# Kernel tuning notes

Hardware: AMD Instinct MI355X
Metric: run time of the kernel (lower is better)

Reference implementation:

```python
import jax, jax.numpy as jnp
import numpy as np

B, N, C = 4, 4096, 1024
H, M = 16, 64          # num_heads, num_landmarks
DH = C // H
SCALE = H ** (-0.5)    # faithful to source: num_heads**-0.5
LN_EPS = 1e-5


def setup_inputs() -> dict:
    key = jax.random.key(0)
    ks = jax.random.split(key, 8)
    s = 0.02
    return {
        "x": jax.random.normal(ks[0], (B, N, C), jnp.float32),
        "ln_w": jnp.ones((C,), jnp.float32),
        "ln_b": jnp.zeros((C,), jnp.float32),
        "qkv_w": jax.random.normal(ks[1], (3 * C, C), jnp.float32) * s,
        "qkv_b": jax.random.normal(ks[2], (3 * C,), jnp.float32) * s,
        "gamma_w": jax.random.normal(ks[3], (C, C), jnp.float32) * s,
        "gamma_b": jax.random.normal(ks[4], (C,), jnp.float32) * s,
        "proj_w": jax.random.normal(ks[5], (C, C), jnp.float32) * s,
        "proj_b": jax.random.normal(ks[6], (C,), jnp.float32) * s,
    }


def _iterative_inv(K, n_iter=6):
    # Newton-Schulz pseudo-inverse on [..., M, M]
    Id = jnp.eye(K.shape[-1], dtype=K.dtype)
    KA = jnp.abs(K)
    V0 = KA.sum(axis=-2, keepdims=True).max(axis=-1, keepdims=True)
    VI = KA.sum(axis=-1, keepdims=True).max(axis=-2, keepdims=True)
    V = jnp.swapaxes(K, -2, -1) / (V0 * VI)
    for _ in range(n_iter):
        KV = K @ V
        V = 0.25 * V @ (13.0 * Id - KV @ (15.0 * Id - KV @ (7.0 * Id - KV)))
    return V


def reference(x, ln_w, ln_b, qkv_w, qkv_b, gamma_w, gamma_b, proj_w, proj_b):
    # LayerNorm
    mu = x.mean(axis=-1, keepdims=True)
    var = x.var(axis=-1, keepdims=True)
    xn = (x - mu) * jax.lax.rsqrt(var + LN_EPS) * ln_w + ln_b
    # qkv: (B,N,3C) -> (3,B,H,N,DH)
    qkv = (xn @ qkv_w.T + qkv_b).reshape(B, N, 3, H, DH).transpose(2, 0, 3, 1, 4)
    q, k, v = qkv[0], qkv[1], qkv[2]
    # landmarks: mean-pool segments of length N//M, then scale
    q_lm = q.reshape(B, H, M, N // M, DH).mean(axis=-2) * SCALE  # (B,H,M,DH)
    k_lm = k.reshape(B, H, M, N // M, DH).mean(axis=-2) * SCALE
    attn1 = jax.nn.softmax(jnp.einsum('bhnd,bhmd->bhnm', q, k_lm), axis=-1)    # (B,H,N,M)
    attn2 = jax.nn.softmax(jnp.einsum('bhmd,bhld->bhml', q_lm, k_lm), axis=-1)  # (B,H,M,M)
    attn3 = jax.nn.softmax(jnp.einsum('bhmd,bhnd->bhmn', q_lm, k), axis=-1)    # (B,H,M,N)
    attn2_inv = _iterative_inv(attn2)
    out = attn1 @ (attn2_inv @ (attn3 @ v))            # (B,H,N,DH)
    out = out.transpose(0, 2, 1, 3).reshape(B, N, C)
    out = out @ gamma_w.T + gamma_b                    # LipNorm=True branch
    out = out @ proj_w.T + proj_b                      # proj (dropout p=0 is identity)
    return out
```

## Files before the change

kernel.cpp:

```cpp
#include <hip/hip_runtime.h>
#include <stdint.h>

typedef unsigned short u16;
typedef short bf16x8 __attribute__((ext_vector_type(8)));
typedef float f32x4 __attribute__((ext_vector_type(4)));

#define MFMA16(a, b, c) __builtin_amdgcn_mfma_f32_16x16x32_bf16((a), (b), (c), 0, 0, 0)

static __device__ __forceinline__ float bfu2f(u16 u) {
  union { unsigned int i; float f; } z; z.i = ((unsigned int)u) << 16; return z.f;
}
static __device__ __forceinline__ u16 f2bfu(float f) {
  union { float f; unsigned int i; } z; z.f = f;
  unsigned int i = z.i;
  return (u16)((i + 0x7fffu + ((i >> 16) & 1u)) >> 16);
}

__device__ __forceinline__ void gload_lds16(const void* g, void* l) {
  __builtin_amdgcn_global_load_lds((const __attribute__((address_space(1))) void*)g,
                                   (__attribute__((address_space(3))) void*)l, 16, 0, 0);
}

__global__ __launch_bounds__(256) void prep_kernel(
    const float* __restrict__ x, const float* __restrict__ lw,
    const float* __restrict__ lb, u16* __restrict__ xn,
    const float* __restrict__ qkvw, u16* __restrict__ QKVW,
    const float* __restrict__ projw, u16* __restrict__ PW,
    const float* __restrict__ G, u16* __restrict__ GT) {
  int blk = blockIdx.x;
  int t = threadIdx.x;
  if (blk < 16384) {
    int row = blk;
    const float4* xr = (const float4*)(x + (size_t)row * 1024);
    float4 v = xr[t];
    float s = v.x + v.y + v.z + v.w;
    float ss = v.x * v.x + v.y * v.y + v.z * v.z + v.w * v.w;
#pragma unroll
    for (int m = 1; m < 64; m <<= 1) { s += __shfl_xor(s, m); ss += __shfl_xor(ss, m); }
    __shared__ float sb[4], ssb[4];
    int lane = t & 63, wvi = t >> 6;
    if (lane == 0) { sb[wvi] = s; ssb[wvi] = ss; }
    __syncthreads();
    s = sb[0] + sb[1] + sb[2] + sb[3];
    ss = ssb[0] + ssb[1] + ssb[2] + ssb[3];
    float mu = s * (1.0f / 1024.0f);
    float var = ss * (1.0f / 1024.0f) - mu * mu;
    float rstd = rsqrtf(var + 1e-5f);
    float4 wv4 = ((const float4*)lw)[t];
    float4 bv4 = ((const float4*)lb)[t];
    ushort4 o;
    o.x = f2bfu((v.x - mu) * rstd * wv4.x + bv4.x);
    o.y = f2bfu((v.y - mu) * rstd * wv4.y + bv4.y);
    o.z = f2bfu((v.z - mu) * rstd * wv4.z + bv4.z);
    o.w = f2bfu((v.w - mu) * rstd * wv4.w + bv4.w);
    ((ushort4*)xn)[(size_t)row * 256 + t] = o;
  } else if (blk < 18432) {
    int idx = (blk - 16384) * 256 + t;
    for (int i = idx; i < 1048576; i += 524288) {
      int j = i << 2;
      const float* s2; u16* d; int off;
      if (j < 3145728) { s2 = qkvw; d = QKVW; off = j; }
      else             { s2 = projw; d = PW; off = j - 3145728; }
      float4 v = *(const float4*)(s2 + off);
      ushort4 o;
      o.x = f2bfu(v.x); o.y = f2bfu(v.y); o.z = f2bfu(v.z); o.w = f2bfu(v.w);
      *(ushort4*)(d + off) = o;
    }
  } else {
    __shared__ float tt[64][65];
    int tg = blk - 18432;
    int tr = (tg >> 4) * 64, tc = (tg & 15) * 64;
    int l = t & 63, y = t >> 6;
    for (int r = y; r < 64; r += 4)
      tt[r][l] = G[(size_t)(tr + r) * 1024 + tc + l];
    __syncthreads();
    for (int rr = y; rr < 64; rr += 4)
      GT[(size_t)(tc + rr) * 1024 + tr + l] = f2bfu(tt[l][rr]);
  }
}

template <int MODE>
__global__ __launch_bounds__(512, 2) void gemm_bt(
    const u16* __restrict__ A, const u16* __restrict__ Bw,
    const float* __restrict__ bias,
    float* __restrict__ Cf, u16* __restrict__ Cb,
    u16* __restrict__ Qo, u16* __restrict__ Ko, u16* __restrict__ Vo,
    int M, int N, int K) {
  __shared__ __attribute__((aligned(16))) u16 As[2][16384];
  __shared__ __attribute__((aligned(16))) u16 Bs[2][16384];
  int tid = threadIdx.x;
  int lane = tid & 63;
  int w = tid >> 6;
  int wr = w >> 2, wc = w & 3;
  int r16 = lane & 15, hi = lane >> 4;
  int l8 = lane >> 3, li = lane & 7;

  int nwg = gridDim.x * gridDim.y;
  int flat = blockIdx.y * gridDim.x + blockIdx.x;
  int q8 = nwg >> 3;
  int swz = (flat & 7) * q8 + (flat >> 3);
  int bx = swz % gridDim.x, by = swz / gridDim.x;

  const char* Abase = (const char*)(A + (size_t)by * 256 * K);
  const char* Bbase = (const char*)(Bw + (size_t)bx * 256 * K);
  size_t rowbytes = (size_t)K * 2;
  int colsw = (li ^ l8) << 4;
  int nkt = K >> 6;

  f32x4 z4 = {0.f, 0.f, 0.f, 0.f};
  f32x4 acc[8][4];
#pragma unroll
  for (int m = 0; m < 8; ++m)
#pragma unroll
    for (int n = 0; n < 4; ++n) acc[m][n] = z4;

#define SG_A(buf, t, r0)                                                      \
  gload_lds16(Abase + (size_t)((r0) + w * 8 + l8) * rowbytes + ((t) << 7) +   \
                  colsw,                                                      \
              (char*)As[buf] + ((r0) + w * 8) * 128)
#define SG_B(buf, t, r0)                                                      \
  gload_lds16(Bbase + (size_t)((r0) + w * 8 + l8) * rowbytes + ((t) << 7) +   \
                  colsw,                                                      \
              (char*)Bs[buf] + ((r0) + w * 8) * 128)

  SG_A(0, 0, 0); SG_A(0, 0, 64); SG_A(0, 0, 128); SG_A(0, 0, 192);
  SG_B(0, 0, 0); SG_B(0, 0, 64); SG_B(0, 0, 128); SG_B(0, 0, 192);
  SG_A(1, 1, 0); SG_A(1, 1, 128); SG_B(1, 1, 0); SG_B(1, 1, 64);
  SG_A(1, 1, 64); SG_A(1, 1, 192);
  asm volatile("s_waitcnt vmcnt(6)" ::: "memory");
  __builtin_amdgcn_s_barrier();
  __builtin_amdgcn_sched_barrier(0);

  int buf = 0;
  bf16x8 af[4][2], bfr[4][2];

#define LDA(mh)                                                               \
  _Pragma("unroll") for (int m = 0; m < 4; ++m) {                             \
    int row = wr * 128 + (mh) * 64 + m * 16 + r16;                            \
    int sw = (row & 7) << 4;                                                  \
    _Pragma("unroll") for (int kk = 0; kk < 2; ++kk)                          \
        af[m][kk] = *(const bf16x8*)(ab + row * 128 +                         \
                                     (((kk << 6) | (hi << 4)) ^ sw));         \
  }
#define LDB(nh)                                                               \
  _Pragma("unroll") for (int n = 0; n < 2; ++n) {                             \
    int row = wc * 64 + (nh) * 32 + n * 16 + r16;                             \
    int sw = (row & 7) << 4;                                                  \
    _Pragma("unroll") for (int kk = 0; kk < 2; ++kk)                          \
        bfr[(nh) * 2 + n][kk] = *(const bf16x8*)(ab2 + row * 128 +            \
                                     (((kk << 6) | (hi << 4)) ^ sw));         \
  }
#define MM(mh, nh)                                                            \
  __builtin_amdgcn_s_setprio(1);                                              \
  _Pragma("unroll") for (int kk = 0; kk < 2; ++kk)                            \
      _Pragma("unroll") for (int m = 0; m < 4; ++m)                           \
          _Pragma("unroll") for (int n = 0; n < 2; ++n)                       \
              acc[(mh) * 4 + m][(nh) * 2 + n] =                               \
      MFMA16(af[m][kk], bfr[(nh) * 2 + n][kk], acc[(mh) * 4 + m][(nh) * 2 + n]); \
  __builtin_amdgcn_s_setprio(0)

#define SBAR __builtin_amdgcn_sched_barrier(0)
#define BAR1                                                                  \
  __builtin_amdgcn_s_barrier();                                               \
  SBAR
#define BAR2                                                                  \
  SBAR;                                                                       \
  __builtin_amdgcn_s_barrier();                                               \
  SBAR

  for (int t = 0; t < nkt; ++t) {
    const char* ab = (const char*)As[buf];
    const char* ab2 = (const char*)Bs[buf];
    bool s1 = (t + 1 < nkt), s2 = (t + 2 < nkt);
    LDA(0);
    LDB(0);
    if (s1) { SG_B(buf ^ 1, t + 1, 128); SG_B(buf ^ 1, t + 1, 192); }
    BAR1;
    MM(0, 0);
    SBAR;
    LDB(1);
    BAR2;
    if (s2) { SG_A(buf, t + 2, 0); SG_A(buf, t + 2, 128); }
    BAR1;
    MM(0, 1);
    SBAR;
    LDA(1);
    BAR2;
    if (s2) { SG_B(buf, t + 2, 0); SG_B(buf, t + 2, 64); }
    BAR1;
    MM(1, 0);
    BAR2;
    if (s2) { SG_A(buf, t + 2, 64); SG_A(buf, t + 2, 192); }
    BAR1;
    MM(1, 1);
    SBAR;
    if (s2) {
      asm volatile("s_waitcnt vmcnt(6)" ::: "memory");
    } else {
      asm volatile("s_waitcnt vmcnt(0)" ::: "memory");
    }
    __builtin_amdgcn_s_barrier();
    SBAR;
    buf ^= 1;
  }
#undef SG_A
#undef SG_B
#undef LDA
#undef LDB
#undef MM
#undef BAR1
#undef BAR2
#undef SBAR

#pragma unroll
  for (int m = 0; m < 8; ++m)
#pragma unroll
    for (int n = 0; n < 4; ++n) {
      int row0 = by * 256 + wr * 128 + m * 16 + hi * 4;
      int col = bx * 256 + wc * 64 + n * 16 + r16;
      if (MODE == 2) {
        int jt = col >> 10;
        int h = (col >> 6) & 15, dh = col & 63;
        int bb = row0 >> 12, nt0 = row0 & 4095;
        float bcol = bias[col];
        if (jt == 2) {
          ushort4 o;
          o.x = f2bfu(acc[m][n][0] + bcol);
          o.y = f2bfu(acc[m][n][1] + bcol);
          o.z = f2bfu(acc[m][n][2] + bcol);
          o.w = f2bfu(acc[m][n][3] + bcol);
          *(ushort4*)&Vo[(((size_t)bb * 16 + h) * 64 + dh) * 4096 + nt0] = o;
        } else {
          u16* dst = (jt == 0) ? Qo : Ko;
#pragma unroll
          for (int r = 0; r < 4; ++r)
            dst[(((size_t)bb * 16 + h) * 4096 + nt0 + r) * 64 + dh] =
                f2bfu(acc[m][n][r] + bcol);
        }
      } else {
        float bcol = bias[col];
#pragma unroll
        for (int r = 0; r < 4; ++r) {
          int row = row0 + r;
          Cf[(size_t)row * N + col] = acc[m][n][r] + bcol;
        }
      }
    }
}

__global__ __launch_bounds__(256) void w2_kernel(
    const u16* __restrict__ A, const u16* __restrict__ Bw,
    float* __restrict__ Cp) {
  __shared__ __attribute__((aligned(16))) u16 As[8192];
  __shared__ __attribute__((aligned(16))) u16 Bs[8192];
  int tid = threadIdx.x, lane = tid & 63, w = tid >> 6;
  int wr = w >> 1, wc = w & 1;
  int r16 = lane & 15, hi = lane >> 4;
  int l8 = lane >> 3, li = lane & 7;
  int bx = blockIdx.x, by = blockIdx.y, kz = blockIdx.z;
  const char* Abase = (const char*)(A + (size_t)by * 131072 + kz * 256);
  const char* Bbase = (const char*)(Bw + (size_t)bx * 131072 + kz * 256);
  int colsw = (li ^ l8) << 4;
  f32x4 z4 = {0.f, 0.f, 0.f, 0.f};
  f32x4 acc[4][4];
#pragma unroll
  for (int m = 0; m < 4; ++m)
#pragma unroll
    for (int n = 0; n < 4; ++n) acc[m][n] = z4;

  for (int kt = 0; kt < 4; ++kt) {
    int kb = kt << 7;
#pragma unroll
    for (int i = 0; i < 4; ++i) {
      int c = w * 4 + i;
      int rr = c * 8 + l8;
      gload_lds16(Abase + (size_t)rr * 2048 + kb + colsw, (char*)As + c * 1024);
      gload_lds16(Bbase + (size_t)rr * 2048 + kb + colsw, (char*)Bs + c * 1024);
    }
    __syncthreads();
    int sw = (lane & 7) << 4;
#pragma unroll
    for (int kk = 0; kk < 2; ++kk) {
      int kby = (kk << 6) + (hi << 4);
      bf16x8 af[4], bfr[4];
#pragma unroll
      for (int m = 0; m < 4; ++m) {
        int row = wr * 64 + m * 16 + r16;
        af[m] = *(const bf16x8*)((const char*)As + row * 128 + (kby ^ sw));
      }
#pragma unroll
      for (int n = 0; n < 4; ++n) {
        int row = wc * 64 + n * 16 + r16;
        bfr[n] = *(const bf16x8*)((const char*)Bs + row * 128 + (kby ^ sw));
      }
#pragma unroll
      for (int m = 0; m < 4; ++m)
#pragma unroll
        for (int n = 0; n < 4; ++n) acc[m][n] = MFMA16(af[m], bfr[n], acc[m][n]);
    }
    __syncthreads();
  }
#pragma unroll
  for (int m = 0; m < 4; ++m)
#pragma unroll
    for (int n = 0; n < 4; ++n)
#pragma unroll
      for (int r = 0; r < 4; ++r) {
        int row = by * 128 + wr * 64 + m * 16 + hi * 4 + r;
        int col = bx * 128 + wc * 64 + n * 16 + r16;
        Cp[(size_t)kz * 1048576 + (size_t)row * 1024 + col] = acc[m][n][r];
      }
}

__global__ __launch_bounds__(256) void w2_reduce_kernel(
    const float* __restrict__ Cp, u16* __restrict__ W2b,
    const float* __restrict__ P, const float* __restrict__ gb,
    const float* __restrict__ pb, float* __restrict__ b2) {
  if (blockIdx.x < 1024) {
    int idx4 = blockIdx.x * 256 + threadIdx.x;
    const float4* p = (const float4*)Cp + idx4;
    float4 s = p[0];
    float4 b = p[262144], c = p[524288], d = p[786432];
    s.x += b.x + c.x + d.x;
    s.y += b.y + c.y + d.y;
    s.z += b.z + c.z + d.z;
    s.w += b.w + c.w + d.w;
    ushort4 o;
    o.x = f2bfu(s.x); o.y = f2bfu(s.y); o.z = f2bfu(s.z); o.w = f2bfu(s.w);
    ((ushort4*)W2b)[idx4] = o;
  } else {
    int i = (blockIdx.x - 1024) * 256 + threadIdx.x;
    const float4* pr = (const float4*)(P + (size_t)i * 1024);
    const float4* g4 = (const float4*)gb;
    float s = 0.f;
    for (int k = 0; k < 256; ++k) {
      float4 a = pr[k], b = g4[k];
      s += a.x * b.x + a.y * b.y + a.z * b.z + a.w * b.w;
    }
    b2[i] = s + pb[i];
  }
}

__global__ __launch_bounds__(64) void landmark_kernel(
    const u16* __restrict__ Q, const u16* __restrict__ K,
    float* __restrict__ qlmf, u16* __restrict__ qlmb,
    float* __restrict__ klmf, u16* __restrict__ klmb) {
  int bm = blockIdx.x;
  int bh = bm >> 6, m = bm & 63;
  int l = threadIdx.x;
  const u16* src = blockIdx.y ? K : Q;
  const u16* base = src + (((size_t)bh * 4096) + m * 64) * 64;
  int r0 = l >> 3;
  int c0 = (l & 7) * 8;
  float s[8] = {};
#pragma unroll
  for (int p = 0; p < 8; ++p) {
    bf16x8 v = *(const bf16x8*)(base + (size_t)(r0 + p * 8) * 64 + c0);
#pragma unroll
    for (int j = 0; j < 8; ++j) s[j] += bfu2f((u16)v[j]);
  }
#pragma unroll
  for (int j = 0; j < 8; ++j) {
    s[j] += __shfl_xor(s[j], 8);
    s[j] += __shfl_xor(s[j], 16);
    s[j] += __shfl_xor(s[j], 32);
  }
  if (l < 8) {
    size_t o = (size_t)bh * 4096 + m * 64 + l * 8;
    float* fo = blockIdx.y ? klmf : qlmf;
    u16* bo = blockIdx.y ? klmb : qlmb;
#pragma unroll
    for (int j = 0; j < 8; ++j) {
      float val = s[j] * (0.25f / 64.0f);
      fo[o + j] = val;
      bo[o + j] = f2bfu(val);
    }
  }
}

__global__ __launch_bounds__(256) void attn3_pv_kernel(
    const u16* __restrict__ qlmb, const u16* __restrict__ Kmat,
    const u16* __restrict__ Vt, float* __restrict__ Upart,
    float* __restrict__ rspart) {
  __shared__ __attribute__((aligned(16))) u16 Elds[4][8192];
  int chunk = blockIdx.x, bh = blockIdx.y;
  int tid = threadIdx.x, lane = tid & 63, w = tid >> 6;
  int r16 = lane & 15, hi = lane >> 4;
  const u16* vtb = Vt + (size_t)bh * 262144;
  const u16* qb = qlmb + (size_t)bh * 4096;
  u16* eb = &Elds[w][0];
  f32x4 z4 = {0.f, 0.f, 0.f, 0.f};

  bf16x8 afr[4][2];
#pragma unroll
  for (int m = 0; m < 4; ++m)
#pragma unroll
    for (int kk = 0; kk < 2; ++kk)
      afr[m][kk] = *(const bf16x8*)(qb + (m * 16 + r16) * 64 + kk * 32 + hi * 8);

  float rs[4][4] = {};
  f32x4 U[4][4];
#pragma unroll
  for (int m = 0; m < 4; ++m)
#pragma unroll
    for (int df = 0; df < 4; ++df) U[m][df] = z4;

  for (int bat = 0; bat < 2; ++bat) {
    int keybase = chunk * 1024 + bat * 512 + w * 128;
    const u16* kb = Kmat + ((size_t)bh * 4096 + keybase) * 64;
    for (int cf = 0; cf < 8; ++cf) {
      f32x4 S[4] = {z4, z4, z4, z4};
#pragma unroll
      for (int kk = 0; kk < 2; ++kk) {
        bf16x8 bfr = *(const bf16x8*)(kb + (size_t)(cf * 16 + r16) * 64 + kk * 32 + hi * 8);
#pragma unroll
        for (int m = 0; m < 4; ++m) S[m] = MFMA16(afr[m][kk], bfr, S[m]);
      }
#pragma unroll
      for (int m = 0; m < 4; ++m)
#pragma unroll
        for (int r = 0; r < 4; ++r) {
          float e = __expf(S[m][r]);
          rs[m][r] += e;
          int row = m * 16 + hi * 4 + r;
          int key = cf * 16 + r16;
          *(u16*)((char*)eb + row * 256 + ((key * 2) ^ ((row & 7) << 4))) = f2bfu(e);
        }
    }
    __syncthreads();
    for (int ks = 0; ks < 4; ++ks) {
      bf16x8 ea[4];
#pragma unroll
      for (int m = 0; m < 4; ++m) {
        int row = m * 16 + r16;
        ea[m] = *(const bf16x8*)((char*)eb + row * 256 + (((ks * 32 + hi * 8) * 2) ^ ((row & 7) << 4)));
      }
#pragma unroll
      for (int df = 0; df < 4; ++df) {
        bf16x8 vb8 = *(const bf16x8*)(vtb + (size_t)(df * 16 + r16) * 4096 +
                                      keybase + ks * 32 + hi * 8);
#pragma unroll
        for (int m = 0; m < 4; ++m) U[m][df] = MFMA16(ea[m], vb8, U[m][df]);
      }
    }
    __syncthreads();
  }

#pragma unroll
  for (int m = 0; m < 4; ++m)
#pragma unroll
    for (int r = 0; r < 4; ++r) {
      float v = rs[m][r];
      v += __shfl_xor(v, 1); v += __shfl_xor(v, 2);
      v += __shfl_xor(v, 4); v += __shfl_xor(v, 8);
      rs[m][r] = v;
    }
  if (r16 == 0) {
    float* rp = rspart + (((size_t)bh * 4 + chunk) * 4 + w) * 64;
#pragma unroll
    for (int m = 0; m < 4; ++m)
#pragma unroll
      for (int r = 0; r < 4; ++r) rp[m * 16 + hi * 4 + r] = rs[m][r];
  }
  float* up = Upart + (((size_t)bh * 4 + chunk) * 4 + w) * 4096;
#pragma unroll
  for (int m = 0; m < 4; ++m)
#pragma unroll
    for (int df = 0; df < 4; ++df)
#pragma unroll
      for (int r = 0; r < 4; ++r)
        up[(m * 16 + hi * 4 + r) * 64 + df * 16 + r16] = U[m][df][r];
}

__global__ __launch_bounds__(256) void reduce_t_kernel(
    const float* __restrict__ Upart, const float* __restrict__ rspart,
    float* __restrict__ Tmf) {
  int bh = blockIdx.y;
  int tid = threadIdx.x;
  __shared__ float rsum[64];
  if (tid < 64) {
    float s = 0.f;
    const float* rp = rspart + (size_t)bh * 1024 + tid;
#pragma unroll 8
    for (int p = 0; p < 16; ++p) s += rp[p * 64];
    rsum[tid] = s;
  }
  __syncthreads();
  int idx4 = blockIdx.x * 256 + tid;
  const float4* up = (const float4*)(Upart + (size_t)bh * 65536) + idx4;
  float4 s = {0.f, 0.f, 0.f, 0.f};
#pragma unroll 8
  for (int p = 0; p < 16; ++p) {
    float4 v = up[p * 1024];
    s.x += v.x; s.y += v.y; s.z += v.z; s.w += v.w;
  }
  float inv = 1.0f / rsum[idx4 >> 4];
  s.x *= inv; s.y *= inv; s.z *= inv; s.w *= inv;
  ((float4*)(Tmf + (size_t)bh * 4096))[idx4] = s;
}

__device__ __forceinline__ void mm64d(const float (*AT)[68], const float (*Bm)[68],
                                      float (*C)[68], float (*CT)[68],
                                      float alpha, float dconst, bool dmode,
                                      int tid) {
  int tr = (tid >> 4) << 2;
  int tc = (tid & 15) << 2;
  float acc[4][4] = {};
#pragma unroll 4
  for (int k = 0; k < 64; ++k) {
    float4 av = *(const float4*)&AT[k][tr];
    float4 bv = *(const float4*)&Bm[k][tc];
    float aa[4] = {av.x, av.y, av.z, av.w};
    float bb[4] = {bv.x, bv.y, bv.z, bv.w};
#pragma unroll
    for (int i = 0; i < 4; ++i)
#pragma unroll
      for (int j = 0; j < 4; ++j) acc[i][j] = fmaf(aa[i], bb[j], acc[i][j]);
  }
#pragma unroll
  for (int i = 0; i < 4; ++i)
#pragma unroll
    for (int j = 0; j < 4; ++j) {
      float raw = acc[i][j] * alpha;
      if (CT) CT[tc + j][tr + i] = raw;
      C[tr + i][tc + j] =
          dmode ? (((tr + i) == (tc + j)) ? dconst - raw : -raw) : raw;
    }
}

__global__ __launch_bounds__(256) void combine_ns_kernel(
    const float* __restrict__ Tmf, const float* __restrict__ qlmf,
    const float* __restrict__ klmf, u16* __restrict__ WT) {
  __shared__ __attribute__((aligned(16))) float A2T[64][68];
  __shared__ __attribute__((aligned(16))) float Vv[64][68];
  __shared__ __attribute__((aligned(16))) float VT[64][68];
  __shared__ __attribute__((aligned(16))) float KV[64][68];
  __shared__ __attribute__((aligned(16))) float KVT[64][68];
  __shared__ __attribute__((aligned(16))) float T2[64][68];
  __shared__ __attribute__((aligned(16))) float T4[64][68];
  __shared__ __attribute__((aligned(16))) float Tm[64][68];
  __shared__ float redbuf[64];
  __shared__ float v0s, scal;
  int bh = blockIdx.x, tid = threadIdx.x;

  for (int idx = tid; idx < 1024; idx += 256) {
    float4 v = ((const float4*)(Tmf + (size_t)bh * 4096))[idx];
    int r = idx >> 4, c0 = (idx & 15) << 2;
    *(float4*)&Tm[r][c0] = v;
  }
  for (int idx = tid; idx < 4096; idx += 256) {
    int r = idx >> 6, c = idx & 63;
    Vv[c][r] = qlmf[(size_t)bh * 4096 + idx];
    VT[c][r] = klmf[(size_t)bh * 4096 + idx];
  }
  __syncthreads();
  mm64d(&Vv[0], &VT[0], &T2[0], nullptr, 1.0f, 0.f, false, tid);
  __syncthreads();
  if (tid < 64) {
    float mx = -1e30f;
    for (int c2 = 0; c2 < 64; ++c2) mx = fmaxf(mx, T2[tid][c2]);
    float s = 0.f;
    for (int c2 = 0; c2 < 64; ++c2) { float e = __expf(T2[tid][c2] - mx); T2[tid][c2] = e; s += e; }
    float inv = 1.f / s;
    for (int c2 = 0; c2 < 64; ++c2) { float p = T2[tid][c2] * inv; T2[tid][c2] = p; A2T[c2][tid] = p; }
  }
  __syncthreads();
  if (tid < 64) {
    float cs = 0.f;
    for (int r2 = 0; r2 < 64; ++r2) cs += fabsf(T2[r2][tid]);
    redbuf[tid] = cs;
  }
  __syncthreads();
  if (tid == 0) {
    float v0 = 0.f;
    for (int c2 = 0; c2 < 64; ++c2) v0 = fmaxf(v0, redbuf[c2]);
    v0s = v0;
  }
  __syncthreads();
  if (tid < 64) {
    float rs2 = 0.f;
    for (int c2 = 0; c2 < 64; ++c2) rs2 += fabsf(T2[tid][c2]);
    redbuf[tid] = rs2;
  }
  __syncthreads();
  if (tid == 0) {
    float vi = 0.f;
    for (int r2 = 0; r2 < 64; ++r2) vi = fmaxf(vi, redbuf[r2]);
    scal = 1.0f / (v0s * vi);
  }
  __syncthreads();
  for (int idx = tid; idx < 4096; idx += 256) {
    int r = idx >> 6, c = idx & 63;
    Vv[r][c] = A2T[r][c] * scal;
    VT[r][c] = T2[r][c] * scal;
  }
  __syncthreads();
  float (*Vt_r)[68] = VT;
  float (*Vt_w)[68] = KV;
#pragma unroll 1
  for (int it = 0; it < 6; ++it) {
    mm64d(&A2T[0], &Vv[0], &T2[0], &KVT[0], 1.0f, 7.0f, true, tid);
    __syncthreads();
    mm64d(&KVT[0], &T2[0], &T4[0], nullptr, 1.0f, 15.0f, true, tid);
    __syncthreads();
    mm64d(&KVT[0], &T4[0], &T2[0], nullptr, 1.0f, 13.0f, true, tid);
    __syncthreads();
    mm64d(Vt_r, &T2[0], &Vv[0], Vt_w, 0.25f, 0.f, false, tid);
    __syncthreads();
    float (*tmp)[68] = Vt_r; Vt_r = Vt_w; Vt_w = tmp;
  }
  mm64d(Vt_r, &Tm[0], &T2[0], nullptr, 1.0f, 0.f, false, tid);
  __syncthreads();
  for (int idx = tid; idx < 4096; idx += 256) {
    int r = idx >> 6, c = idx & 63;
    WT[(size_t)bh * 4096 + c * 64 + r] = f2bfu(T2[r][c]);
  }
}

__global__ __launch_bounds__(256) void attn1_out_kernel(
    const u16* __restrict__ Q, const u16* __restrict__ klmb,
    const u16* __restrict__ WT, u16* __restrict__ AO) {
  __shared__ __attribute__((aligned(16))) u16 Elds[4][2048];
  int bh = blockIdx.y;
  int b = bh >> 4, h = bh & 15;
  int tid = threadIdx.x, lane = tid & 63, w = tid >> 6;
  int r16 = lane & 15, hi = lane >> 4;
  int rowbase = blockIdx.x * 128 + w * 32;
  const u16* qb = Q + ((size_t)bh * 4096 + rowbase) * 64;
  const u16* kb = klmb + (size_t)bh * 4096;
  const u16* wtb = WT + (size_t)bh * 4096;
  u16* eb = &Elds[w][0];
  f32x4 z4 = {0.f, 0.f, 0.f, 0.f};

  bf16x8 afr[2][2];
#pragma unroll
  for (int mi = 0; mi < 2; ++mi)
#pragma unroll
    for (int kk = 0; kk < 2; ++kk)
      afr[mi][kk] = *(const bf16x8*)(qb + (mi * 16 + r16) * 64 + kk * 32 + hi * 8);

  float rs[2][4] = {};
  for (int cf = 0; cf < 4; ++cf) {
    f32x4 S[2] = {z4, z4};
#pragma unroll
    for (int kk = 0; kk < 2; ++kk) {
      bf16x8 bfr = *(const bf16x8*)(kb + (cf * 16 + r16) * 64 + kk * 32 + hi * 8);
#pragma unroll
      for (int mi = 0; mi < 2; ++mi) S[mi] = MFMA16(afr[mi][kk], bfr, S[mi]);
    }
#pragma unroll
    for (int mi = 0; mi < 2; ++mi)
#pragma unroll
      for (int r = 0; r < 4; ++r) {
        float e = __expf(S[mi][r]);
        rs[mi][r] += e;
        int row = mi * 16 + hi * 4 + r;
        int key = cf * 16 + r16;
        *(u16*)((char*)eb + row * 128 + ((key * 2) ^ ((row & 7) << 4))) = f2bfu(e);
      }
  }
#pragma unroll
  for (int mi = 0; mi < 2; ++mi)
#pragma unroll
    for (int r = 0; r < 4; ++r) {
      float v = rs[mi][r];
      v += __shfl_xor(v, 1); v += __shfl_xor(v, 2);
      v += __shfl_xor(v, 4); v += __shfl_xor(v, 8);
      rs[mi][r] = v;
    }
  __syncthreads();

  f32x4 O[2][4];
#pragma unroll
  for (int mi = 0; mi < 2; ++mi)
#pragma unroll
    for (int df = 0; df < 4; ++df) O[mi][df] = z4;
  for (int ks = 0; ks < 2; ++ks) {
    bf16x8 ea[2];
#pragma unroll
    for (int mi = 0; mi < 2; ++mi) {
      int row = mi * 16 + r16;
      ea[mi] = *(const bf16x8*)((char*)eb + row * 128 + (((ks * 32 + hi * 8) * 2) ^ ((row & 7) << 4)));
    }
#pragma unroll
    for (int df = 0; df < 4; ++df) {
      bf16x8 wfr = *(const bf16x8*)(wtb + (df * 16 + r16) * 64 + ks * 32 + hi * 8);
#pragma unroll
      for (int mi = 0; mi < 2; ++mi) O[mi][df] = MFMA16(ea[mi], wfr, O[mi][df]);
    }
  }
#pragma unroll
  for (int mi = 0; mi < 2; ++mi)
#pragma unroll
    for (int df = 0; df < 4; ++df)
#pragma unroll
      for (int r = 0; r < 4; ++r) {
        int row = mi * 16 + hi * 4 + r;
        int n = rowbase + row;
        int col = h * 64 + df * 16 + r16;
        float val = O[mi][df][r] / rs[mi][r];
        AO[((size_t)b * 4096 + n) * 1024 + col] = f2bfu(val);
      }
}

extern "C" void kernel_launch(void* const* d_in, const int* in_sizes, int n_in,
                              void* d_out, int out_size, void* d_ws, size_t ws_size,
                              hipStream_t stream) {
  (void)in_sizes; (void)n_in; (void)out_size; (void)ws_size;
  const float* x       = (const float*)d_in[0];
  const float* ln_w    = (const float*)d_in[1];
  const float* ln_b    = (const float*)d_in[2];
  const float* qkv_w   = (const float*)d_in[3];
  const float* qkv_b   = (const float*)d_in[4];
  const float* gamma_w = (const float*)d_in[5];
  const float* gamma_b = (const float*)d_in[6];
  const float* proj_w  = (const float*)d_in[7];
  const float* proj_b  = (const float*)d_in[8];

  char* ws = (char*)d_ws;
  u16* XN     = (u16*)(ws + 0);
  u16* Qb     = (u16*)(ws + 33554432);
  u16* Kb     = (u16*)(ws + 67108864);
  u16* Vb     = (u16*)(ws + 100663296);
  u16* QKVW   = (u16*)(ws + 134217728);
  u16* GTb    = (u16*)(ws + 140509184);
  u16* PW     = (u16*)(ws + 142606336);
  float* QLMF = (float*)(ws + 144703488);
  float* KLMF = (float*)(ws + 145752064);
  u16* QLMB   = (u16*)(ws + 146800640);
  u16* KLMB   = (u16*)(ws + 147324928);
  float* RSP  = (float*)(ws + 147849216);
  u16* WTb    = (u16*)(ws + 148373504);
  float* UP   = (float*)XN;
  float* CPF  = (float*)(ws + 16777216);
  float* TMF  = (float*)Kb;
  u16* W2b    = (u16*)(ws + 102760448);
  float* B2F  = (float*)(ws + 104857600);

  prep_kernel<<<18688, 256, 0, stream>>>(x, ln_w, ln_b, XN,
                                         qkv_w, QKVW, proj_w, PW, gamma_w, GTb);
  gemm_bt<2><<<dim3(12, 64), 512, 0, stream>>>(XN, QKVW, qkv_b, nullptr, nullptr,
                                               Qb, Kb, Vb, 16384, 3072, 1024);
  landmark_kernel<<<dim3(4096, 2), 64, 0, stream>>>(Qb, Kb, QLMF, QLMB, KLMF, KLMB);
  attn3_pv_kernel<<<dim3(4, 64), 256, 0, stream>>>(QLMB, Kb, Vb, UP, RSP);
  reduce_t_kernel<<<dim3(4, 64), 256, 0, stream>>>(UP, RSP, TMF);
  w2_kernel<<<dim3(8, 8, 4), 256, 0, stream>>>(PW, GTb, CPF);
  w2_reduce_kernel<<<1028, 256, 0, stream>>>(CPF, W2b, proj_w, gamma_b, proj_b, B2F);
  combine_ns_kernel<<<64, 256, 0, stream>>>(TMF, QLMF, KLMF, WTb);
  attn1_out_kernel<<<dim3(32, 64), 256, 0, stream>>>(Qb, KLMB, WTb, XN);
  gemm_bt<1><<<dim3(4, 64), 512, 0, stream>>>(XN, W2b, B2F, (float*)d_out, nullptr,
                                              nullptr, nullptr, nullptr, 16384, 1024, 1024);
}
```

Baseline: 371.0 us.

## Merge small side kernels into existing launches to cut launch count

The standalone w2 GEMM (proj_w x gamma_w) now runs as extra blocks inside attn3_pv_kernel, and its split-K reduction runs as extra blocks inside combine_ns_kernel. The bias-folding dot products move into prep_kernel, and the reduce_t step is folded into the start of combine_ns_kernel. This removes three kernel launches and lets the small side work overlap with the main attention work. In exchange it adds block-index branching, shares LDS across unrelated work, and reorders barriers in the main GEMM loop.

```diff
diff --git a/kernel.cpp b/kernel.cpp
--- a/kernel.cpp
+++ b/kernel.cpp
@@ -26,7 +26,9 @@
     const float* __restrict__ lb, u16* __restrict__ xn,
     const float* __restrict__ qkvw, u16* __restrict__ QKVW,
     const float* __restrict__ projw, u16* __restrict__ PW,
-    const float* __restrict__ G, u16* __restrict__ GT) {
+    const float* __restrict__ G, u16* __restrict__ GT,
+    const float* __restrict__ gb, const float* __restrict__ pb,
+    float* __restrict__ b2) {
   int blk = blockIdx.x;
   int t = threadIdx.x;
   if (blk < 16384) {
@@ -66,7 +68,7 @@
       o.x = f2bfu(v.x); o.y = f2bfu(v.y); o.z = f2bfu(v.z); o.w = f2bfu(v.w);
       *(ushort4*)(d + off) = o;
     }
-  } else {
+  } else if (blk < 18688) {
     __shared__ float tt[64][65];
     int tg = blk - 18432;
     int tr = (tg >> 4) * 64, tc = (tg & 15) * 64;
@@ -76,6 +78,16 @@
     __syncthreads();
     for (int rr = y; rr < 64; rr += 4)
       GT[(size_t)(tc + rr) * 1024 + tr + l] = f2bfu(tt[l][rr]);
+  } else {
+    int i = (blk - 18688) * 256 + t;
+    const float4* pr = (const float4*)(projw + (size_t)i * 1024);
+    const float4* g4 = (const float4*)gb;
+    float s = 0.f;
+    for (int k = 0; k < 256; ++k) {
+      float4 a = pr[k], b = g4[k];
+      s += a.x * b.x + a.y * b.y + a.z * b.z + a.w * b.w;
+    }
+    b2[i] = s + pb[i];
   }
 }
 
@@ -159,14 +171,13 @@
       MFMA16(af[m][kk], bfr[(nh) * 2 + n][kk], acc[(mh) * 4 + m][(nh) * 2 + n]); \
   __builtin_amdgcn_s_setprio(0)
 
-#define SBAR __builtin_amdgcn_sched_barrier(0)
 #define BAR1                                                                  \
   __builtin_amdgcn_s_barrier();                                               \
-  SBAR
+  __builtin_amdgcn_sched_barrier(0)
 #define BAR2                                                                  \
-  SBAR;                                                                       \
+  __builtin_amdgcn_sched_barrier(0);                                          \
   __builtin_amdgcn_s_barrier();                                               \
-  SBAR
+  __builtin_amdgcn_sched_barrier(0)
 
   for (int t = 0; t < nkt; ++t) {
     const char* ab = (const char*)As[buf];
@@ -177,15 +188,13 @@
     if (s1) { SG_B(buf ^ 1, t + 1, 128); SG_B(buf ^ 1, t + 1, 192); }
     BAR1;
     MM(0, 0);
-    SBAR;
+    BAR2;
     LDB(1);
-    BAR2;
     if (s2) { SG_A(buf, t + 2, 0); SG_A(buf, t + 2, 128); }
     BAR1;
     MM(0, 1);
-    SBAR;
+    BAR2;
     LDA(1);
-    BAR2;
     if (s2) { SG_B(buf, t + 2, 0); SG_B(buf, t + 2, 64); }
     BAR1;
     MM(1, 0);
@@ -193,14 +202,14 @@
     if (s2) { SG_A(buf, t + 2, 64); SG_A(buf, t + 2, 192); }
     BAR1;
     MM(1, 1);
-    SBAR;
+    __builtin_amdgcn_sched_barrier(0);
     if (s2) {
       asm volatile("s_waitcnt vmcnt(6)" ::: "memory");
     } else {
       asm volatile("s_waitcnt vmcnt(0)" ::: "memory");
     }
     __builtin_amdgcn_s_barrier();
-    SBAR;
+    __builtin_amdgcn_sched_barrier(0);
     buf ^= 1;
   }
 #undef SG_A
@@ -210,7 +219,6 @@
 #undef MM
 #undef BAR1
 #undef BAR2
-#undef SBAR
 
 #pragma unroll
   for (int m = 0; m < 8; ++m)
@@ -248,99 +256,6 @@
     }
 }
 
-__global__ __launch_bounds__(256) void w2_kernel(
-    const u16* __restrict__ A, const u16* __restrict__ Bw,
-    float* __restrict__ Cp) {
-  __shared__ __attribute__((aligned(16))) u16 As[8192];
-  __shared__ __attribute__((aligned(16))) u16 Bs[8192];
-  int tid = threadIdx.x, lane = tid & 63, w = tid >> 6;
-  int wr = w >> 1, wc = w & 1;
-  int r16 = lane & 15, hi = lane >> 4;
-  int l8 = lane >> 3, li = lane & 7;
-  int bx = blockIdx.x, by = blockIdx.y, kz = blockIdx.z;
-  const char* Abase = (const char*)(A + (size_t)by * 131072 + kz * 256);
-  const char* Bbase = (const char*)(Bw + (size_t)bx * 131072 + kz * 256);
-  int colsw = (li ^ l8) << 4;
-  f32x4 z4 = {0.f, 0.f, 0.f, 0.f};
-  f32x4 acc[4][4];
-#pragma unroll
-  for (int m = 0; m < 4; ++m)
-#pragma unroll
-    for (int n = 0; n < 4; ++n) acc[m][n] = z4;
-
-  for (int kt = 0; kt < 4; ++kt) {
-    int kb = kt << 7;
-#pragma unroll
-    for (int i = 0; i < 4; ++i) {
-      int c = w * 4 + i;
-      int rr = c * 8 + l8;
-      gload_lds16(Abase + (size_t)rr * 2048 + kb + colsw, (char*)As + c * 1024);
-      gload_lds16(Bbase + (size_t)rr * 2048 + kb + colsw, (char*)Bs + c * 1024);
-    }
-    __syncthreads();
-    int sw = (lane & 7) << 4;
-#pragma unroll
-    for (int kk = 0; kk < 2; ++kk) {
-      int kby = (kk << 6) + (hi << 4);
-      bf16x8 af[4], bfr[4];
-#pragma unroll
-      for (int m = 0; m < 4; ++m) {
-        int row = wr * 64 + m * 16 + r16;
-        af[m] = *(const bf16x8*)((const char*)As + row * 128 + (kby ^ sw));
-      }
-#pragma unroll
-      for (int n = 0; n < 4; ++n) {
-        int row = wc * 64 + n * 16 + r16;
-        bfr[n] = *(const bf16x8*)((const char*)Bs + row * 128 + (kby ^ sw));
-      }
-#pragma unroll
-      for (int m = 0; m < 4; ++m)
-#pragma unroll
-        for (int n = 0; n < 4; ++n) acc[m][n] = MFMA16(af[m], bfr[n], acc[m][n]);
-    }
-    __syncthreads();
-  }
-#pragma unroll
-  for (int m = 0; m < 4; ++m)
-#pragma unroll
-    for (int n = 0; n < 4; ++n)
-#pragma unroll
-      for (int r = 0; r < 4; ++r) {
-        int row = by * 128 + wr * 64 + m * 16 + hi * 4 + r;
-        int col = bx * 128 + wc * 64 + n * 16 + r16;
-        Cp[(size_t)kz * 1048576 + (size_t)row * 1024 + col] = acc[m][n][r];
-      }
-}
-
-__global__ __launch_bounds__(256) void w2_reduce_kernel(
-    const float* __restrict__ Cp, u16* __restrict__ W2b,
-    const float* __restrict__ P, const float* __restrict__ gb,
-    const float* __restrict__ pb, float* __restrict__ b2) {
-  if (blockIdx.x < 1024) {
-    int idx4 = blockIdx.x * 256 + threadIdx.x;
-    const float4* p = (const float4*)Cp + idx4;
-    float4 s = p[0];
-    float4 b = p[262144], c = p[524288], d = p[786432];
-    s.x += b.x + c.x + d.x;
-    s.y += b.y + c.y + d.y;
-    s.z += b.z + c.z + d.z;
-    s.w += b.w + c.w + d.w;
-    ushort4 o;
-    o.x = f2bfu(s.x); o.y = f2bfu(s.y); o.z = f2bfu(s.z); o.w = f2bfu(s.w);
-    ((ushort4*)W2b)[idx4] = o;
-  } else {
-    int i = (blockIdx.x - 1024) * 256 + threadIdx.x;
-    const float4* pr = (const float4*)(P + (size_t)i * 1024);
-    const float4* g4 = (const float4*)gb;
-    float s = 0.f;
-    for (int k = 0; k < 256; ++k) {
-      float4 a = pr[k], b = g4[k];
-      s += a.x * b.x + a.y * b.y + a.z * b.z + a.w * b.w;
-    }
-    b2[i] = s + pb[i];
-  }
-}
-
 __global__ __launch_bounds__(64) void landmark_kernel(
     const u16* __restrict__ Q, const u16* __restrict__ K,
     float* __restrict__ qlmf, u16* __restrict__ qlmb,
@@ -381,11 +296,75 @@
 __global__ __launch_bounds__(256) void attn3_pv_kernel(
     const u16* __restrict__ qlmb, const u16* __restrict__ Kmat,
     const u16* __restrict__ Vt, float* __restrict__ Upart,
-    float* __restrict__ rspart) {
+    float* __restrict__ rspart,
+    const u16* __restrict__ Aw2, const u16* __restrict__ Bw2,
+    float* __restrict__ Cp) {
   __shared__ __attribute__((aligned(16))) u16 Elds[4][8192];
-  int chunk = blockIdx.x, bh = blockIdx.y;
   int tid = threadIdx.x, lane = tid & 63, w = tid >> 6;
   int r16 = lane & 15, hi = lane >> 4;
+  int l8 = lane >> 3, li = lane & 7;
+
+  if (blockIdx.x >= 4) {
+    int wid = (blockIdx.x - 4) * 64 + blockIdx.y;
+    u16* As = &Elds[0][0];
+    u16* Bs = &Elds[1][0];
+    int wr = w >> 1, wc = w & 1;
+    int kz = wid >> 6, bxw = wid & 7, byw = (wid >> 3) & 7;
+    const char* Abase = (const char*)(Aw2 + (size_t)byw * 131072 + kz * 256);
+    const char* Bbase = (const char*)(Bw2 + (size_t)bxw * 131072 + kz * 256);
+    int colsw = (li ^ l8) << 4;
+    f32x4 z4 = {0.f, 0.f, 0.f, 0.f};
+    f32x4 acc[4][4];
+#pragma unroll
+    for (int m = 0; m < 4; ++m)
+#pragma unroll
+      for (int n = 0; n < 4; ++n) acc[m][n] = z4;
+    for (int kt = 0; kt < 4; ++kt) {
+      int kb = kt << 7;
+#pragma unroll
+      for (int i = 0; i < 4; ++i) {
+        int c = w * 4 + i;
+        int rr = c * 8 + l8;
+        gload_lds16(Abase + (size_t)rr * 2048 + kb + colsw, (char*)As + c * 1024);
+        gload_lds16(Bbase + (size_t)rr * 2048 + kb + colsw, (char*)Bs + c * 1024);
+      }
+      __syncthreads();
+      int sw = (lane & 7) << 4;
+#pragma unroll
+      for (int kk = 0; kk < 2; ++kk) {
+        int kby = (kk << 6) + (hi << 4);
+        bf16x8 af[4], bfr[4];
+#pragma unroll
+        for (int m = 0; m < 4; ++m) {
+          int row = wr * 64 + m * 16 + r16;
+          af[m] = *(const bf16x8*)((const char*)As + row * 128 + (kby ^ sw));
+        }
+#pragma unroll
+        for (int n = 0; n < 4; ++n) {
+          int row = wc * 64 + n * 16 + r16;
+          bfr[n] = *(const bf16x8*)((const char*)Bs + row * 128 + (kby ^ sw));
+        }
+#pragma unroll
+        for (int m = 0; m < 4; ++m)
+#pragma unroll
+          for (int n = 0; n < 4; ++n) acc[m][n] = MFMA16(af[m], bfr[n], acc[m][n]);
+      }
+      __syncthreads();
+    }
+#pragma unroll
+    for (int m = 0; m < 4; ++m)
+#pragma unroll
+      for (int n = 0; n < 4; ++n)
+#pragma unroll
+        for (int r = 0; r < 4; ++r) {
+          int row = byw * 128 + wr * 64 + m * 16 + hi * 4 + r;
+          int col = bxw * 128 + wc * 64 + n * 16 + r16;
+          Cp[(size_t)kz * 1048576 + (size_t)row * 1024 + col] = acc[m][n][r];
+        }
+    return;
+  }
+
+  int chunk = blockIdx.x, bh = blockIdx.y;
   const u16* vtb = Vt + (size_t)bh * 262144;
   const u16* qb = qlmb + (size_t)bh * 4096;
   u16* eb = &Elds[w][0];
@@ -470,33 +449,6 @@
 #pragma unroll
       for (int r = 0; r < 4; ++r)
         up[(m * 16 + hi * 4 + r) * 64 + df * 16 + r16] = U[m][df][r];
-}
-
-__global__ __launch_bounds__(256) void reduce_t_kernel(
-    const float* __restrict__ Upart, const float* __restrict__ rspart,
-    float* __restrict__ Tmf) {
-  int bh = blockIdx.y;
-  int tid = threadIdx.x;
-  __shared__ float rsum[64];
-  if (tid < 64) {
-    float s = 0.f;
-    const float* rp = rspart + (size_t)bh * 1024 + tid;
-#pragma unroll 8
-    for (int p = 0; p < 16; ++p) s += rp[p * 64];
-    rsum[tid] = s;
-  }
-  __syncthreads();
-  int idx4 = blockIdx.x * 256 + tid;
-  const float4* up = (const float4*)(Upart + (size_t)bh * 65536) + idx4;
-  float4 s = {0.f, 0.f, 0.f, 0.f};
-#pragma unroll 8
-  for (int p = 0; p < 16; ++p) {
-    float4 v = up[p * 1024];
-    s.x += v.x; s.y += v.y; s.z += v.z; s.w += v.w;
-  }
-  float inv = 1.0f / rsum[idx4 >> 4];
-  s.x *= inv; s.y *= inv; s.z *= inv; s.w *= inv;
-  ((float4*)(Tmf + (size_t)bh * 4096))[idx4] = s;
 }
 
 __device__ __forceinline__ void mm64d(const float (*AT)[68], const float (*Bm)[68],
@@ -521,16 +473,33 @@
   for (int i = 0; i < 4; ++i)
 #pragma unroll
     for (int j = 0; j < 4; ++j) {
-      float raw = acc[i][j] * alpha;
-      if (CT) CT[tc + j][tr + i] = raw;
+      float vv = acc[i][j] * alpha;
+      if (CT) CT[tc + j][tr + i] = vv;
       C[tr + i][tc + j] =
-          dmode ? (((tr + i) == (tc + j)) ? dconst - raw : -raw) : raw;
+          dmode ? (((tr + i) == (tc + j)) ? dconst - vv : -vv) : vv;
     }
 }
 
 __global__ __launch_bounds__(256) void combine_ns_kernel(
-    const float* __restrict__ Tmf, const float* __restrict__ qlmf,
-    const float* __restrict__ klmf, u16* __restrict__ WT) {
+    const float* __restrict__ Upart, const float* __restrict__ rspart,
+    const float* __restrict__ qlmf, const float* __restrict__ klmf,
+    u16* __restrict__ WT, const float* __restrict__ Cp,
+    u16* __restrict__ W2b) {
+  int tid = threadIdx.x;
+  if (blockIdx.x >= 64) {
+    int idx4 = (blockIdx.x - 64) * 256 + tid;
+    const float4* p = (const float4*)Cp + idx4;
+    float4 s = p[0];
+    float4 b = p[262144], c = p[524288], d = p[786432];
+    s.x += b.x + c.x + d.x;
+    s.y += b.y + c.y + d.y;
+    s.z += b.z + c.z + d.z;
+    s.w += b.w + c.w + d.w;
+    ushort4 o;
+    o.x = f2bfu(s.x); o.y = f2bfu(s.y); o.z = f2bfu(s.z); o.w = f2bfu(s.w);
+    ((ushort4*)W2b)[idx4] = o;
+    return;
+  }
   __shared__ __attribute__((aligned(16))) float A2T[64][68];
   __shared__ __attribute__((aligned(16))) float Vv[64][68];
   __shared__ __attribute__((aligned(16))) float VT[64][68];
@@ -539,14 +508,30 @@
   __shared__ __attribute__((aligned(16))) float T2[64][68];
   __shared__ __attribute__((aligned(16))) float T4[64][68];
   __shared__ __attribute__((aligned(16))) float Tm[64][68];
-  __shared__ float redbuf[64];
+  __shared__ float rsum[64], redbuf[64];
   __shared__ float v0s, scal;
-  int bh = blockIdx.x, tid = threadIdx.x;
-
-  for (int idx = tid; idx < 1024; idx += 256) {
-    float4 v = ((const float4*)(Tmf + (size_t)bh * 4096))[idx];
-    int r = idx >> 4, c0 = (idx & 15) << 2;
-    *(float4*)&Tm[r][c0] = v;
+  int bh = blockIdx.x;
+
+  if (tid < 64) {
+    float s = 0.f;
+    const float* rp = rspart + (size_t)bh * 1024 + tid;
+#pragma unroll 8
+    for (int p = 0; p < 16; ++p) s += rp[p * 64];
+    rsum[tid] = s;
+  }
+  __syncthreads();
+  for (int idx4 = tid; idx4 < 1024; idx4 += 256) {
+    const float4* up = (const float4*)(Upart + (size_t)bh * 65536) + idx4;
+    float4 s = {0.f, 0.f, 0.f, 0.f};
+#pragma unroll 8
+    for (int p = 0; p < 16; ++p) {
+      float4 v = up[p * 1024];
+      s.x += v.x; s.y += v.y; s.z += v.z; s.w += v.w;
+    }
+    float inv = 1.0f / rsum[idx4 >> 4];
+    int r = idx4 >> 4, c0 = (idx4 & 15) << 2;
+    Tm[r][c0] = s.x * inv; Tm[r][c0 + 1] = s.y * inv;
+    Tm[r][c0 + 2] = s.z * inv; Tm[r][c0 + 3] = s.w * inv;
   }
   for (int idx = tid; idx < 4096; idx += 256) {
     int r = idx >> 6, c = idx & 63;
@@ -730,23 +715,21 @@
   u16* QLMB   = (u16*)(ws + 146800640);
   u16* KLMB   = (u16*)(ws + 147324928);
   float* RSP  = (float*)(ws + 147849216);
+  float* B2F  = (float*)(ws + 148111360);
   u16* WTb    = (u16*)(ws + 148373504);
   float* UP   = (float*)XN;
   float* CPF  = (float*)(ws + 16777216);
-  float* TMF  = (float*)Kb;
   u16* W2b    = (u16*)(ws + 102760448);
-  float* B2F  = (float*)(ws + 104857600);
-
-  prep_kernel<<<18688, 256, 0, stream>>>(x, ln_w, ln_b, XN,
-                                         qkv_w, QKVW, proj_w, PW, gamma_w, GTb);
+
+  prep_kernel<<<18692, 256, 0, stream>>>(x, ln_w, ln_b, XN, qkv_w, QKVW,
+                                         proj_w, PW, gamma_w, GTb,
+                                         gamma_b, proj_b, B2F);
   gemm_bt<2><<<dim3(12, 64), 512, 0, stream>>>(XN, QKVW, qkv_b, nullptr, nullptr,
                                                Qb, Kb, Vb, 16384, 3072, 1024);
   landmark_kernel<<<dim3(4096, 2), 64, 0, stream>>>(Qb, Kb, QLMF, QLMB, KLMF, KLMB);
-  attn3_pv_kernel<<<dim3(4, 64), 256, 0, stream>>>(QLMB, Kb, Vb, UP, RSP);
-  reduce_t_kernel<<<dim3(4, 64), 256, 0, stream>>>(UP, RSP, TMF);
-  w2_kernel<<<dim3(8, 8, 4), 256, 0, stream>>>(PW, GTb, CPF);
-  w2_reduce_kernel<<<1028, 256, 0, stream>>>(CPF, W2b, proj_w, gamma_b, proj_b, B2F);
-  combine_ns_kernel<<<64, 256, 0, stream>>>(TMF, QLMF, KLMF, WTb);
+  attn3_pv_kernel<<<dim3(8, 64), 256, 0, stream>>>(QLMB, Kb, Vb, UP, RSP,
+                                                   PW, GTb, CPF);
+  combine_ns_kernel<<<1088, 256, 0, stream>>>(UP, RSP, QLMF, KLMF, WTb, CPF, W2b);
   attn1_out_kernel<<<dim3(32, 64), 256, 0, stream>>>(Qb, KLMB, WTb, XN);
   gemm_bt<1><<<dim3(4, 64), 512, 0, stream>>>(XN, W2b, B2F, (float*)d_out, nullptr,
                                               nullptr, nullptr, nullptr, 16384, 1024, 1024);
```

Result: no change. 375.1 us (+1.1%).
